# Performance work log

Hardware: AMD Instinct MI355X
Metric: run time of the kernel (lower is better)

Reference implementation:

```python
import jax, jax.numpy as jnp
import numpy as np

B, S, HID = 2, 2048, 2048
N_HEADS, N_KV, HD = 32, 8, 64
ROPE_BASE = 10000.0


def setup_inputs() -> dict:
    key = jax.random.key(0)
    k1, k2, k3 = jax.random.split(key, 3)
    hidden_states = jax.random.normal(k1, (B, S, HID), dtype=jnp.float32)
    position_ids = jnp.broadcast_to(jnp.arange(S, dtype=jnp.int32), (B, S))
    # additive causal mask [B, 1, S, S]
    causal = jnp.where(jnp.tril(jnp.ones((S, S), dtype=bool)), 0.0, -1e9).astype(jnp.float32)
    attention_mask = jnp.broadcast_to(causal[None, None], (B, 1, S, S))
    qkv_w = jax.random.normal(k2, (HID, N_HEADS * HD + 2 * N_KV * HD), dtype=jnp.float32) * 0.02
    o_w = jax.random.normal(k3, (HID, HID), dtype=jnp.float32) * 0.02
    return {"hidden_states": hidden_states, "position_ids": position_ids,
            "attention_mask": attention_mask, "qkv_w": qkv_w, "o_w": o_w}


def _rotate_half(x):
    x1, x2 = jnp.split(x, 2, axis=-1)
    return jnp.concatenate([-x2, x1], axis=-1)


def reference(hidden_states, position_ids, attention_mask, qkv_w, o_w):
    b, s, _ = hidden_states.shape
    qkv = hidden_states @ qkv_w  # [B,S,3072]
    q_pos = N_HEADS * HD
    kv_pos = N_KV * HD
    q = qkv[..., :q_pos].reshape(b, s, N_HEADS, HD).transpose(0, 2, 1, 3)       # [B,H,S,D]
    k = qkv[..., q_pos:q_pos + kv_pos].reshape(b, s, N_KV, HD).transpose(0, 2, 1, 3)  # [B,Hkv,S,D]
    v = qkv[..., q_pos + kv_pos:].reshape(b, s, N_KV, HD).transpose(0, 2, 1, 3)       # [B,Hkv,S,D]

    # rotary embedding (TFPhi3RotaryEmbedding)
    inv_freq = 1.0 / (ROPE_BASE ** (jnp.arange(0, HD, 2, dtype=jnp.float32) / HD))  # [D/2]
    freqs = position_ids.astype(jnp.float32)[:, :, None] * inv_freq[None, None, :]  # [B,S,D/2]
    emb = jnp.concatenate([freqs, freqs], axis=-1)  # [B,S,D]
    cos = jnp.cos(emb)[:, None]  # [B,1,S,D]
    sin = jnp.sin(emb)[:, None]
    q = q * cos + _rotate_half(q) * sin
    k = k * cos + _rotate_half(k) * sin

    # GQA: repeat_kv with n_rep = 4 (repeat_interleave over head dim)
    n_rep = N_HEADS // N_KV
    k = jnp.repeat(k, n_rep, axis=1)  # [B,H,S,D]
    v = jnp.repeat(v, n_rep, axis=1)

    scores = jnp.einsum('bhqd,bhkd->bhqk', q, k) / np.sqrt(HD).astype(np.float32)
    scores = scores + attention_mask
    weights = jax.nn.softmax(scores, axis=-1)
    attn = jnp.einsum('bhqk,bhkd->bhqd', weights, v)  # [B,H,S,D]
    attn = attn.transpose(0, 2, 1, 3).reshape(b, s, HID)
    return attn @ o_w
```

## Files before the change

### kernel.cpp

```cpp
#include <hip/hip_runtime.h>
#include <stdint.h>


typedef unsigned short u16;
typedef __bf16 bf16x8 __attribute__((ext_vector_type(8)));
typedef float f32x4 __attribute__((ext_vector_type(4)));
typedef unsigned short u16x8 __attribute__((ext_vector_type(8)));
typedef unsigned int u32x4 __attribute__((ext_vector_type(4)));

__device__ __forceinline__ u16 f2bf(float f) {
  unsigned int u = __float_as_uint(f);
  u += 0x7fffu + ((u >> 16) & 1u);
  return (u16)(u >> 16);
}

__device__ __forceinline__ unsigned cvt_pk_bf16(float lo, float hi) {
  unsigned r;
  asm("v_cvt_pk_bf16_f32 %0, %1, %2" : "=v"(r) : "v"(lo), "v"(hi));
  return r;
}

__device__ __forceinline__ void gload_lds16(const void* g, void* l) {
  __builtin_amdgcn_global_load_lds((const __attribute__((address_space(1))) void*)g,
                                   (__attribute__((address_space(3))) void*)l, 16, 0, 0);
}

__global__ __launch_bounds__(256) void conv_bf16_kernel(const float* __restrict__ in,
                                                        u16* __restrict__ out, int n8) {
  int i = blockIdx.x * 256 + threadIdx.x;
  int stride = gridDim.x * 256;
  for (; i < n8; i += stride) {
    const float4* p = (const float4*)in + (size_t)i * 2;
    float4 a = p[0], b = p[1];
    u16x8 o;
    o[0] = f2bf(a.x); o[1] = f2bf(a.y); o[2] = f2bf(a.z); o[3] = f2bf(a.w);
    o[4] = f2bf(b.x); o[5] = f2bf(b.y); o[6] = f2bf(b.z); o[7] = f2bf(b.w);
    *(u16x8*)(out + (size_t)i * 8) = o;
  }
}

__global__ __launch_bounds__(256) void wtrans_kernel(const float* __restrict__ in,
                                                     u16* __restrict__ out, int R, int C) {
  __shared__ float tile[32][33];
  int tx = threadIdx.x & 31, ty = threadIdx.x >> 5;
  int col = blockIdx.x * 32 + tx;
  for (int j = ty; j < 32; j += 8)
    tile[j][tx] = in[(size_t)(blockIdx.y * 32 + j) * C + col];
  __syncthreads();
  int ocol = blockIdx.y * 32 + tx;
  for (int j = ty; j < 32; j += 8)
    out[(size_t)(blockIdx.x * 32 + j) * R + ocol] = f2bf(tile[tx][j]);
}

__global__ __launch_bounds__(256) void rope_table_kernel(float* __restrict__ cost,
                                                         float* __restrict__ sint) {
  int idx = blockIdx.x * 256 + threadIdx.x;
  if (idx >= 2048 * 32) return;
  int p = idx >> 5, i = idx & 31;
  float invf = powf(10000.f, -(float)i / 32.f);
  float ang = (float)p * invf;
  cost[idx] = cosf(ang);
  sint[idx] = sinf(ang);
}

__global__ __launch_bounds__(256) void gemm_bt_kernel(const u16* __restrict__ A,
                                                      const u16* __restrict__ Bt,
                                                      float* __restrict__ C,
                                                      int M, int N, int K) {
  __shared__ __align__(16) u16 lds_a[128 * 32];
  __shared__ __align__(16) u16 lds_b[128 * 32];
  const int tid = threadIdx.x;
  const int lane = tid & 63;
  const int w = tid >> 6;
  const int wr = w >> 1, wc = w & 1;
  const int brow = blockIdx.y * 128;
  const int bcol = blockIdx.x * 128;

  f32x4 acc[4][4] = {};

  const int off0 = w * 2048 + lane * 16;

  for (int kt = 0; kt < K; kt += 32) {
#pragma unroll
    for (int i = 0; i < 2; ++i) {
      int off = off0 + i * 1024;
      int r = off >> 6;
      int ce = (off & 63) >> 1;
      gload_lds16(A + (size_t)(brow + r) * K + kt + ce,
                  lds_a + ((w * 2048 + i * 1024) >> 1));
      gload_lds16(Bt + (size_t)(bcol + r) * K + kt + ce,
                  lds_b + ((w * 2048 + i * 1024) >> 1));
    }
    __syncthreads();

    bf16x8 a[4], b[4];
#pragma unroll
    for (int m = 0; m < 4; ++m)
      a[m] = *(const bf16x8*)&lds_a[(wr * 64 + m * 16 + (lane & 15)) * 32 + (lane >> 4) * 8];
#pragma unroll
    for (int n = 0; n < 4; ++n)
      b[n] = *(const bf16x8*)&lds_b[(wc * 64 + n * 16 + (lane & 15)) * 32 + (lane >> 4) * 8];
#pragma unroll
    for (int m = 0; m < 4; ++m)
#pragma unroll
      for (int n = 0; n < 4; ++n)
        acc[m][n] = __builtin_amdgcn_mfma_f32_16x16x32_bf16(a[m], b[n], acc[m][n], 0, 0, 0);
    __syncthreads();
  }

#pragma unroll
  for (int m = 0; m < 4; ++m) {
    int row0 = brow + wr * 64 + m * 16 + (lane >> 4) * 4;
#pragma unroll
    for (int n = 0; n < 4; ++n) {
      int col = bcol + wc * 64 + n * 16 + (lane & 15);
#pragma unroll
      for (int j = 0; j < 4; ++j)
        C[(size_t)(row0 + j) * N + col] = acc[m][n][j];
    }
  }
}

__global__ __launch_bounds__(256) void rope_scatter_kernel(const float* __restrict__ qkv,
                                                           const int* __restrict__ pos_ids,
                                                           const float* __restrict__ cost,
                                                           const float* __restrict__ sint,
                                                           u16* __restrict__ Qo,
                                                           u16* __restrict__ Ko) {
  int t = blockIdx.x;
  int b = t >> 11, s = t & 2047;
  int pos = pos_ids[t];
  const float* row = qkv + (size_t)t * 3072;
  int tid = threadIdx.x;
  const float QSCALE = 0.125f * 1.44269504088896340736f;

  for (int idx = tid; idx < 1024; idx += 256) {
    int hh = idx >> 5, i = idx & 31;
    float x1 = row[hh * 64 + i], x2 = row[hh * 64 + i + 32];
    float c = cost[pos * 32 + i], sn = sint[pos * 32 + i];
    float o1 = (x1 * c - x2 * sn) * QSCALE;
    float o2 = (x2 * c + x1 * sn) * QSCALE;
    size_t base = ((size_t)(b * 32 + hh) * 2048 + s) * 64;
    Qo[base + i] = f2bf(o1);
    Qo[base + i + 32] = f2bf(o2);
  }
  {
    int hh = tid >> 5, i = tid & 31;
    float x1 = row[2048 + hh * 64 + i], x2 = row[2048 + hh * 64 + i + 32];
    float c = cost[pos * 32 + i], sn = sint[pos * 32 + i];
    float o1 = x1 * c - x2 * sn;
    float o2 = x2 * c + x1 * sn;
    size_t base = ((size_t)(b * 8 + hh) * 2048 + s) * 64;
    Ko[base + i] = f2bf(o1);
    Ko[base + i + 32] = f2bf(o2);
  }
}

__global__ __launch_bounds__(256) void vtrans_kernel(const float* __restrict__ qkv,
                                                     u16* __restrict__ Vt) {
  __shared__ float tile[64][65];
  int b = blockIdx.x >> 3, hv = blockIdx.x & 7;
  int s0 = blockIdx.y * 64;
  int tid = threadIdx.x;
  for (int idx = tid; idx < 4096; idx += 256) {
    int tok = idx >> 6, c = idx & 63;
    tile[tok][c] = qkv[(size_t)(b * 2048 + s0 + tok) * 3072 + 2560 + hv * 64 + c];
  }
  __syncthreads();
  size_t obase = (size_t)(b * 8 + hv) * 64 * 2048;
  for (int idx = tid; idx < 4096; idx += 256) {
    int d = idx >> 6, si = idx & 63;
    Vt[obase + (size_t)d * 2048 + s0 + si] = f2bf(tile[si][d]);
  }
}

__global__ __launch_bounds__(256) void attn_kernel(const u16* __restrict__ Q,
                                                   const u16* __restrict__ Kk,
                                                   const u16* __restrict__ Vt,
                                                   u16* __restrict__ O) {
  __shared__ __align__(16) u16 lds_k[64 * 64];
  __shared__ __align__(16) u16 lds_v[64 * 64];

  const int tid = threadIdx.x;
  const int lane = tid & 63;
  const int w = tid >> 6;
  const int g = lane >> 4;
  const int q = lane & 15;
  const int bh = blockIdx.x;
  const int b = bh >> 5, h = bh & 31, hkv = (bh & 31) >> 2;
  const size_t qbase = (size_t)(b * 32 + h) * 2048 * 64;
  const size_t kbase = (size_t)(b * 8 + hkv) * 2048 * 64;
  const size_t vbase = (size_t)(b * 8 + hkv) * 64 * 2048;
  const int pair = blockIdx.y;

  const int src0 = q | (((2 * g) & 3) << 4);
  const int src1 = q | (((2 * g + 1) & 3) << 4);
  const bool hiN = g >= 2;
  const int srcQ = (lane & 48) | (4 * g);

  for (int half = 0; half < 2; ++half) {
    const int qt = half ? (31 - pair) : pair;
    const int qb = qt * 64;

    bf16x8 aq[2];
    {
      const u16* qp = Q + qbase + (size_t)(qb + w * 16 + q) * 64 + g * 8;
      aq[0] = *(const bf16x8*)(qp);
      aq[1] = *(const bf16x8*)(qp + 32);
    }

    f32x4 oacc[4] = {};
    float m = -1e30f, l = 0.f;

    for (int kt = 0; kt <= qt; ++kt) {
      const int k0 = kt * 64;
#pragma unroll
      for (int i = 0; i < 2; ++i) {
        int off = w * 2048 + i * 1024 + lane * 16;
        int sw = off ^ (((off >> 7) & 7) << 4);
        int r = sw >> 7;
        int ce = (sw & 127) >> 1;
        gload_lds16(Kk + kbase + (size_t)(k0 + r) * 64 + ce,
                    lds_k + ((w * 2048 + i * 1024) >> 1));
        gload_lds16(Vt + vbase + (size_t)r * 2048 + k0 + ce,
                    lds_v + ((w * 2048 + i * 1024) >> 1));
      }
      __syncthreads();

      const bool diag = (kt == qt);
      const int nmax = diag ? w : 3;

      f32x4 sacc[4] = {};
#pragma unroll
      for (int n = 0; n < 4; ++n) {
        if (n > nmax) break;
        int row = n * 16 + q;
#pragma unroll
        for (int c = 0; c < 2; ++c) {
          int byte = row * 128 + c * 64 + g * 16;
          byte ^= ((row & 7) << 4);
          bf16x8 ak = *(const bf16x8*)&lds_k[byte >> 1];
          sacc[n] = __builtin_amdgcn_mfma_f32_16x16x32_bf16(ak, aq[c], sacc[n], 0, 0, 0);
        }
      }

      if (diag) {
#pragma unroll
        for (int n = 0; n < 4; ++n)
#pragma unroll
          for (int j = 0; j < 4; ++j)
            if (n * 16 + 4 * g + j > w * 16 + q) sacc[n][j] = -1e30f;
      }

      float mx = sacc[0][0];
#pragma unroll
      for (int n = 0; n < 4; ++n)
#pragma unroll
        for (int j = 0; j < 4; ++j) mx = fmaxf(mx, sacc[n][j]);
      mx = fmaxf(mx, __shfl_xor(mx, 16, 64));
      mx = fmaxf(mx, __shfl_xor(mx, 32, 64));
      float mnew = fmaxf(m, mx);
      float alpha = exp2f(m - mnew);
      m = mnew;

      float p[4][4];
      float rs = 0.f;
#pragma unroll
      for (int n = 0; n < 4; ++n)
#pragma unroll
        for (int j = 0; j < 4; ++j) {
          float pv = exp2f(sacc[n][j] - mnew);
          p[n][j] = pv;
          rs += pv;
        }
      rs += __shfl_xor(rs, 16, 64);
      rs += __shfl_xor(rs, 32, 64);
      l = l * alpha + rs;

#pragma unroll
      for (int j = 0; j < 4; ++j) {
        float aj = __shfl(alpha, srcQ + j, 64);
#pragma unroll
        for (int n = 0; n < 4; ++n) oacc[n][j] *= aj;
      }

      unsigned pk[4][2];
#pragma unroll
      for (int n = 0; n < 4; ++n) {
        pk[n][0] = cvt_pk_bf16(p[n][0], p[n][1]);
        pk[n][1] = cvt_pk_bf16(p[n][2], p[n][3]);
      }

#pragma unroll
      for (int c = 0; c < 2; ++c) {
        if (diag && w < 2 && c == 1) break;
        u32x4 wv;
        {
          int t0 = __shfl((int)pk[2 * c][0], src0, 64);
          int t1 = __shfl((int)pk[2 * c + 1][0], src0, 64);
          wv[0] = (unsigned)(hiN ? t1 : t0);
          t0 = __shfl((int)pk[2 * c][1], src0, 64);
          t1 = __shfl((int)pk[2 * c + 1][1], src0, 64);
          wv[1] = (unsigned)(hiN ? t1 : t0);
          t0 = __shfl((int)pk[2 * c][0], src1, 64);
          t1 = __shfl((int)pk[2 * c + 1][0], src1, 64);
          wv[2] = (unsigned)(hiN ? t1 : t0);
          t0 = __shfl((int)pk[2 * c][1], src1, 64);
          t1 = __shfl((int)pk[2 * c + 1][1], src1, 64);
          wv[3] = (unsigned)(hiN ? t1 : t0);
        }
        bf16x8 pa = __builtin_bit_cast(bf16x8, wv);
#pragma unroll
        for (int n = 0; n < 4; ++n) {
          int row = n * 16 + q;
          int byte = row * 128 + c * 64 + g * 16;
          byte ^= ((row & 7) << 4);
          bf16x8 bv = *(const bf16x8*)&lds_v[byte >> 1];
          oacc[n] = __builtin_amdgcn_mfma_f32_16x16x32_bf16(pa, bv, oacc[n], 0, 0, 0);
        }
      }
      __syncthreads();
    }

    float linv[4];
#pragma unroll
    for (int j = 0; j < 4; ++j)
      linv[j] = __builtin_amdgcn_rcpf(__shfl(l, srcQ + j, 64));
#pragma unroll
    for (int n = 0; n < 4; ++n) {
      int col = h * 64 + n * 16 + q;
#pragma unroll
      for (int j = 0; j < 4; ++j) {
        int qrow = qb + w * 16 + 4 * g + j;
        O[(size_t)(b * 2048 + qrow) * 2048 + col] = f2bf(oacc[n][j] * linv[j]);
      }
    }
  }
}

extern "C" void kernel_launch(void* const* d_in, const int* in_sizes, int n_in,
                              void* d_out, int out_size, void* d_ws, size_t ws_size,
                              hipStream_t stream) {
  const float* hidden = (const float*)d_in[0];
  const int* pos = (const int*)d_in[1];
  const float* qkv_w = (const float*)d_in[3];
  const float* o_w = (const float*)d_in[4];
  float* out = (float*)d_out;
  char* ws = (char*)d_ws;

  u16* wqkvT  = (u16*)(ws + 0);
  u16* woT    = (u16*)(ws + 12582912);
  u16* hidb   = (u16*)(ws + 20971520);
  float* qkvbuf = (float*)(ws + 37748736);
  u16* kb     = (u16*)(ws + 88080384);
  u16* vtb    = (u16*)(ws + 92274688);
  float* cost = (float*)(ws + 96468992);
  float* sint = (float*)(ws + 96731136);
  u16* qbuf   = hidb;
  u16* attnb  = (u16*)qkvbuf;

  conv_bf16_kernel<<<4096, 256, 0, stream>>>(hidden, hidb, 1048576);
  wtrans_kernel<<<dim3(96, 64), 256, 0, stream>>>(qkv_w, wqkvT, 2048, 3072);
  wtrans_kernel<<<dim3(64, 64), 256, 0, stream>>>(o_w, woT, 2048, 2048);
  rope_table_kernel<<<256, 256, 0, stream>>>(cost, sint);

  gemm_bt_kernel<<<dim3(24, 32), 256, 0, stream>>>(hidb, wqkvT, qkvbuf, 4096, 3072, 2048);

  rope_scatter_kernel<<<4096, 256, 0, stream>>>(qkvbuf, pos, cost, sint, qbuf, kb);
  vtrans_kernel<<<dim3(16, 32), 256, 0, stream>>>(qkvbuf, vtb);

  attn_kernel<<<dim3(64, 16), 256, 0, stream>>>(qbuf, kb, vtb, attnb);

  gemm_bt_kernel<<<dim3(16, 32), 256, 0, stream>>>(attnb, woT, out, 4096, 2048, 2048);
}
```

Before: 392.3 us.

## Replace GEMM with double-buffered 256x256 tile kernel and pipeline attention KV loads

Replaces the 128x128 GEMM with a 512-thread 256x256-tile kernel that double-buffers 64-wide K slices in LDS, uses XOR swizzling, an XCD-aware block remap, and setprio around the MFMA bursts. The attention kernel now double-buffers K/V tiles so the next tile's loads overlap compute. It also passes P through per-wave LDS instead of the lane shuffles, and uses raw v_exp_f32. The large LDS footprint reduces occupancy, and the GEMM grids shrink to 192 and 128 blocks, which may underfill the GPU.

```diff
diff --git a/kernel.cpp b/kernel.cpp
--- a/kernel.cpp
+++ b/kernel.cpp
@@ -6,7 +6,6 @@
 typedef __bf16 bf16x8 __attribute__((ext_vector_type(8)));
 typedef float f32x4 __attribute__((ext_vector_type(4)));
 typedef unsigned short u16x8 __attribute__((ext_vector_type(8)));
-typedef unsigned int u32x4 __attribute__((ext_vector_type(4)));
 
 __device__ __forceinline__ u16 f2bf(float f) {
   unsigned int u = __float_as_uint(f);
@@ -17,6 +16,12 @@
 __device__ __forceinline__ unsigned cvt_pk_bf16(float lo, float hi) {
   unsigned r;
   asm("v_cvt_pk_bf16_f32 %0, %1, %2" : "=v"(r) : "v"(lo), "v"(hi));
+  return r;
+}
+
+__device__ __forceinline__ float fexp2(float x) {
+  float r;
+  asm("v_exp_f32 %0, %1" : "=v"(r) : "v"(x));
   return r;
 }
 
@@ -63,60 +68,109 @@
   sint[idx] = sinf(ang);
 }
 
-__global__ __launch_bounds__(256) void gemm_bt_kernel(const u16* __restrict__ A,
+__global__ __launch_bounds__(512) void gemm256_kernel(const u16* __restrict__ A,
                                                       const u16* __restrict__ Bt,
                                                       float* __restrict__ C,
                                                       int M, int N, int K) {
-  __shared__ __align__(16) u16 lds_a[128 * 32];
-  __shared__ __align__(16) u16 lds_b[128 * 32];
+  __shared__ __align__(16) char lds[131072];
   const int tid = threadIdx.x;
   const int lane = tid & 63;
   const int w = tid >> 6;
-  const int wr = w >> 1, wc = w & 1;
-  const int brow = blockIdx.y * 128;
-  const int bcol = blockIdx.x * 128;
-
-  f32x4 acc[4][4] = {};
-
-  const int off0 = w * 2048 + lane * 16;
-
-  for (int kt = 0; kt < K; kt += 32) {
-#pragma unroll
-    for (int i = 0; i < 2; ++i) {
-      int off = off0 + i * 1024;
-      int r = off >> 6;
-      int ce = (off & 63) >> 1;
-      gload_lds16(A + (size_t)(brow + r) * K + kt + ce,
-                  lds_a + ((w * 2048 + i * 1024) >> 1));
-      gload_lds16(Bt + (size_t)(bcol + r) * K + kt + ce,
-                  lds_b + ((w * 2048 + i * 1024) >> 1));
-    }
-    __syncthreads();
-
-    bf16x8 a[4], b[4];
-#pragma unroll
-    for (int m = 0; m < 4; ++m)
-      a[m] = *(const bf16x8*)&lds_a[(wr * 64 + m * 16 + (lane & 15)) * 32 + (lane >> 4) * 8];
-#pragma unroll
-    for (int n = 0; n < 4; ++n)
-      b[n] = *(const bf16x8*)&lds_b[(wc * 64 + n * 16 + (lane & 15)) * 32 + (lane >> 4) * 8];
-#pragma unroll
-    for (int m = 0; m < 4; ++m)
-#pragma unroll
-      for (int n = 0; n < 4; ++n)
-        acc[m][n] = __builtin_amdgcn_mfma_f32_16x16x32_bf16(a[m], b[n], acc[m][n], 0, 0, 0);
-    __syncthreads();
-  }
-
-#pragma unroll
-  for (int m = 0; m < 4; ++m) {
-    int row0 = brow + wr * 64 + m * 16 + (lane >> 4) * 4;
-#pragma unroll
-    for (int n = 0; n < 4; ++n) {
-      int col = bcol + wc * 64 + n * 16 + (lane & 15);
+  const int wm = w >> 2, wn = w & 3;
+
+  const int nwg = gridDim.x * gridDim.y;
+  const int flat = blockIdx.y * gridDim.x + blockIdx.x;
+  const int cpx = nwg >> 3;
+  const int swb = (flat & 7) * cpx + (flat >> 3);
+  const int bx = swb % gridDim.x, by = swb / gridDim.x;
+  const int brow = by * 256, bcol = bx * 256;
+
+  const int nt = K >> 6;
+  f32x4 acc[8][4] = {};
+
+  auto stage_tile = [&](int kt, int buf) {
+    char* ab = lds + buf * 65536;
+    char* bb = ab + 32768;
+#pragma unroll
+    for (int hf = 0; hf < 2; ++hf)
+#pragma unroll
+      for (int i = 0; i < 2; ++i) {
+        int P = (w * 2 + i) * 1024 + lane * 16;
+        int L = P ^ (((P >> 9) & 1) << 5);
+        int r = L >> 7, c = (L & 127) >> 1;
+        gload_lds16(A + (size_t)(brow + hf * 128 + r) * K + kt + c,
+                    ab + hf * 16384 + (w * 2 + i) * 1024);
+      }
+#pragma unroll
+    for (int hf = 0; hf < 2; ++hf)
+#pragma unroll
+      for (int i = 0; i < 2; ++i) {
+        int P = (w * 2 + i) * 1024 + lane * 16;
+        int L = P ^ (((P >> 9) & 1) << 5);
+        int r = L >> 7, c = (L & 127) >> 1;
+        gload_lds16(Bt + (size_t)(bcol + hf * 128 + r) * K + kt + c,
+                    bb + hf * 16384 + (w * 2 + i) * 1024);
+      }
+  };
+
+  stage_tile(0, 0);
+
+  for (int t = 0; t < nt; ++t) {
+    const int cur = t & 1;
+    const char* ah = lds + cur * 65536 + wm * 16384;
+    const char* bh = lds + cur * 65536 + 32768 + (wn >> 1) * 16384;
+    const int rb = (wn & 1) * 64;
+
+    if (t + 1 < nt) {
+      stage_tile((t + 1) << 6, cur ^ 1);
+      asm volatile("s_waitcnt vmcnt(8)" ::: "memory");
+    } else {
+      asm volatile("s_waitcnt vmcnt(0)" ::: "memory");
+    }
+    __builtin_amdgcn_s_barrier();
+    asm volatile("" ::: "memory");
+
+#pragma unroll
+    for (int p = 0; p < 4; ++p) {
+      bf16x8 af[2][2], bfr[4][2];
+#pragma unroll
+      for (int i = 0; i < 2; ++i)
+#pragma unroll
+        for (int kk = 0; kk < 2; ++kk) {
+          int lin = ((p * 2 + i) * 16 + (lane & 15)) * 128 + kk * 64 + (lane >> 4) * 16;
+          af[i][kk] = *(const bf16x8*)(ah + (lin ^ (((lin >> 9) & 1) << 5)));
+        }
+#pragma unroll
+      for (int fn = 0; fn < 4; ++fn)
+#pragma unroll
+        for (int kk = 0; kk < 2; ++kk) {
+          int lin = (rb + fn * 16 + (lane & 15)) * 128 + kk * 64 + (lane >> 4) * 16;
+          bfr[fn][kk] = *(const bf16x8*)(bh + (lin ^ (((lin >> 9) & 1) << 5)));
+        }
+      __builtin_amdgcn_s_barrier();
+      __builtin_amdgcn_s_setprio(1);
+#pragma unroll
+      for (int i = 0; i < 2; ++i)
+#pragma unroll
+        for (int fn = 0; fn < 4; ++fn)
+#pragma unroll
+          for (int kk = 0; kk < 2; ++kk)
+            acc[p * 2 + i][fn] = __builtin_amdgcn_mfma_f32_16x16x32_bf16(
+                af[i][kk], bfr[fn][kk], acc[p * 2 + i][fn], 0, 0, 0);
+      __builtin_amdgcn_s_setprio(0);
+      __builtin_amdgcn_s_barrier();
+    }
+  }
+
+#pragma unroll
+  for (int fm = 0; fm < 8; ++fm) {
+    int row0 = brow + wm * 128 + fm * 16 + (lane >> 4) * 4;
+#pragma unroll
+    for (int fn = 0; fn < 4; ++fn) {
+      int col = bcol + wn * 64 + fn * 16 + (lane & 15);
 #pragma unroll
       for (int j = 0; j < 4; ++j)
-        C[(size_t)(row0 + j) * N + col] = acc[m][n][j];
+        C[(size_t)(row0 + j) * N + col] = acc[fm][fn][j];
     }
   }
 }
@@ -178,8 +232,9 @@
                                                    const u16* __restrict__ Kk,
                                                    const u16* __restrict__ Vt,
                                                    u16* __restrict__ O) {
-  __shared__ __align__(16) u16 lds_k[64 * 64];
-  __shared__ __align__(16) u16 lds_v[64 * 64];
+  __shared__ __align__(16) u16 lds_k[2][64 * 64];
+  __shared__ __align__(16) u16 lds_v[2][64 * 64];
+  __shared__ __align__(16) u16 lds_p[4][1024];
 
   const int tid = threadIdx.x;
   const int lane = tid & 63;
@@ -192,11 +247,20 @@
   const size_t kbase = (size_t)(b * 8 + hkv) * 2048 * 64;
   const size_t vbase = (size_t)(b * 8 + hkv) * 64 * 2048;
   const int pair = blockIdx.y;
-
-  const int src0 = q | (((2 * g) & 3) << 4);
-  const int src1 = q | (((2 * g + 1) & 3) << 4);
-  const bool hiN = g >= 2;
   const int srcQ = (lane & 48) | (4 * g);
+
+  auto stageKV = [&](int k0, int buf) {
+#pragma unroll
+    for (int i = 0; i < 2; ++i) {
+      int off = w * 2048 + i * 1024 + lane * 16;
+      int sw2 = off ^ (((off >> 7) & 7) << 4);
+      int r = sw2 >> 7, ce = (sw2 & 127) >> 1;
+      gload_lds16(Kk + kbase + (size_t)(k0 + r) * 64 + ce,
+                  (u16*)lds_k[buf] + ((w * 2048 + i * 1024) >> 1));
+      gload_lds16(Vt + vbase + (size_t)r * 2048 + k0 + ce,
+                  (u16*)lds_v[buf] + ((w * 2048 + i * 1024) >> 1));
+    }
+  };
 
   for (int half = 0; half < 2; ++half) {
     const int qt = half ? (31 - pair) : pair;
@@ -212,20 +276,18 @@
     f32x4 oacc[4] = {};
     float m = -1e30f, l = 0.f;
 
+    stageKV(0, 0);
+
     for (int kt = 0; kt <= qt; ++kt) {
-      const int k0 = kt * 64;
-#pragma unroll
-      for (int i = 0; i < 2; ++i) {
-        int off = w * 2048 + i * 1024 + lane * 16;
-        int sw = off ^ (((off >> 7) & 7) << 4);
-        int r = sw >> 7;
-        int ce = (sw & 127) >> 1;
-        gload_lds16(Kk + kbase + (size_t)(k0 + r) * 64 + ce,
-                    lds_k + ((w * 2048 + i * 1024) >> 1));
-        gload_lds16(Vt + vbase + (size_t)r * 2048 + k0 + ce,
-                    lds_v + ((w * 2048 + i * 1024) >> 1));
-      }
-      __syncthreads();
+      const int cur = kt & 1;
+      if (kt < qt) {
+        stageKV((kt + 1) * 64, cur ^ 1);
+        asm volatile("s_waitcnt vmcnt(4)" ::: "memory");
+      } else {
+        asm volatile("s_waitcnt vmcnt(0)" ::: "memory");
+      }
+      __builtin_amdgcn_s_barrier();
+      asm volatile("" ::: "memory");
 
       const bool diag = (kt == qt);
       const int nmax = diag ? w : 3;
@@ -239,7 +301,7 @@
         for (int c = 0; c < 2; ++c) {
           int byte = row * 128 + c * 64 + g * 16;
           byte ^= ((row & 7) << 4);
-          bf16x8 ak = *(const bf16x8*)&lds_k[byte >> 1];
+          bf16x8 ak = *(const bf16x8*)&lds_k[cur][byte >> 1];
           sacc[n] = __builtin_amdgcn_mfma_f32_16x16x32_bf16(ak, aq[c], sacc[n], 0, 0, 0);
         }
       }
@@ -260,7 +322,7 @@
       mx = fmaxf(mx, __shfl_xor(mx, 16, 64));
       mx = fmaxf(mx, __shfl_xor(mx, 32, 64));
       float mnew = fmaxf(m, mx);
-      float alpha = exp2f(m - mnew);
+      float alpha = fexp2(m - mnew);
       m = mnew;
 
       float p[4][4];
@@ -269,7 +331,7 @@
       for (int n = 0; n < 4; ++n)
 #pragma unroll
         for (int j = 0; j < 4; ++j) {
-          float pv = exp2f(sacc[n][j] - mnew);
+          float pv = fexp2(sacc[n][j] - mnew);
           p[n][j] = pv;
           rs += pv;
         }
@@ -290,36 +352,32 @@
         pk[n][0] = cvt_pk_bf16(p[n][0], p[n][1]);
         pk[n][1] = cvt_pk_bf16(p[n][2], p[n][3]);
       }
+      {
+        char* pbase = (char*)lds_p[w] + q * 128;
+#pragma unroll
+        for (int n = 0; n < 4; ++n) {
+          unsigned long long v =
+              (unsigned long long)pk[n][0] | ((unsigned long long)pk[n][1] << 32);
+          *(unsigned long long*)(pbase + (((2 * n + (g >> 1)) ^ (q & 7)) << 4) +
+                                 ((g & 1) << 3)) = v;
+        }
+      }
 
 #pragma unroll
       for (int c = 0; c < 2; ++c) {
         if (diag && w < 2 && c == 1) break;
-        u32x4 wv;
-        {
-          int t0 = __shfl((int)pk[2 * c][0], src0, 64);
-          int t1 = __shfl((int)pk[2 * c + 1][0], src0, 64);
-          wv[0] = (unsigned)(hiN ? t1 : t0);
-          t0 = __shfl((int)pk[2 * c][1], src0, 64);
-          t1 = __shfl((int)pk[2 * c + 1][1], src0, 64);
-          wv[1] = (unsigned)(hiN ? t1 : t0);
-          t0 = __shfl((int)pk[2 * c][0], src1, 64);
-          t1 = __shfl((int)pk[2 * c + 1][0], src1, 64);
-          wv[2] = (unsigned)(hiN ? t1 : t0);
-          t0 = __shfl((int)pk[2 * c][1], src1, 64);
-          t1 = __shfl((int)pk[2 * c + 1][1], src1, 64);
-          wv[3] = (unsigned)(hiN ? t1 : t0);
-        }
-        bf16x8 pa = __builtin_bit_cast(bf16x8, wv);
+        bf16x8 pa = *(const bf16x8*)((char*)lds_p[w] + q * 128 +
+                                     (((4 * c + g) ^ (q & 7)) << 4));
 #pragma unroll
         for (int n = 0; n < 4; ++n) {
           int row = n * 16 + q;
           int byte = row * 128 + c * 64 + g * 16;
           byte ^= ((row & 7) << 4);
-          bf16x8 bv = *(const bf16x8*)&lds_v[byte >> 1];
+          bf16x8 bv = *(const bf16x8*)&lds_v[cur][byte >> 1];
           oacc[n] = __builtin_amdgcn_mfma_f32_16x16x32_bf16(pa, bv, oacc[n], 0, 0, 0);
         }
       }
-      __syncthreads();
+      __builtin_amdgcn_s_barrier();
     }
 
     float linv[4];
@@ -364,12 +422,12 @@
   wtrans_kernel<<<dim3(64, 64), 256, 0, stream>>>(o_w, woT, 2048, 2048);
   rope_table_kernel<<<256, 256, 0, stream>>>(cost, sint);
 
-  gemm_bt_kernel<<<dim3(24, 32), 256, 0, stream>>>(hidb, wqkvT, qkvbuf, 4096, 3072, 2048);
+  gemm256_kernel<<<dim3(12, 16), 512, 0, stream>>>(hidb, wqkvT, qkvbuf, 4096, 3072, 2048);
 
   rope_scatter_kernel<<<4096, 256, 0, stream>>>(qkvbuf, pos, cost, sint, qbuf, kb);
   vtrans_kernel<<<dim3(16, 32), 256, 0, stream>>>(qkvbuf, vtb);
 
   attn_kernel<<<dim3(64, 16), 256, 0, stream>>>(qbuf, kb, vtb, attnb);
 
-  gemm_bt_kernel<<<dim3(16, 32), 256, 0, stream>>>(attnb, woT, out, 4096, 2048, 2048);
-}
+  gemm256_kernel<<<dim3(8, 16), 512, 0, stream>>>(attnb, woT, out, 4096, 2048, 2048);
+}
```

Result: slower. 431.0 us (+9.9%).
